# Performance work log

Hardware: AMD Instinct MI355X
Metric: run time of the kernel (lower is better)

## Reference

```python
import jax, jax.numpy as jnp
import numpy as np

N_NODES = 50000
N_EDGES = 600000
D_IN = 128
D_HID = 128
D_OUT = 128
LN_EPS = 1e-5


def _layer_norm(h, g, b):
    mu = jnp.mean(h, axis=-1, keepdims=True)
    var = jnp.var(h, axis=-1, keepdims=True)
    return (h - mu) * jax.lax.rsqrt(var + LN_EPS) * g + b


def _gin_conv(x, src, dst, w1, b1, w2, b2):
    # sum-aggregate neighbor messages at destination nodes, eps = 0
    agg = jax.ops.segment_sum(x[src], dst, num_segments=x.shape[0])
    h = x + agg
    h = jax.nn.relu(h @ w1 + b1)
    return h @ w2 + b2


def setup_inputs() -> dict:
    key = jax.random.key(0)
    ks = jax.random.split(key, 20)
    x = jax.random.normal(ks[0], (N_NODES, D_IN), dtype=jnp.float32)
    edge_index = jax.random.randint(ks[1], (2, N_EDGES), 0, N_NODES, dtype=jnp.int64)
    dims = [(D_IN, D_HID), (D_HID, D_HID), (D_HID, D_HID), (D_HID, D_OUT)]
    inp = {"x": x, "edge_index": edge_index}
    for i, (din, dout) in enumerate(dims):
        s1 = 1.0 / np.sqrt(din)
        s2 = 1.0 / np.sqrt(D_HID)
        inp[f"w1_{i}"] = jax.random.uniform(ks[2 + 4 * i], (din, D_HID), jnp.float32, -s1, s1)
        inp[f"b1_{i}"] = jax.random.uniform(ks[3 + 4 * i], (D_HID,), jnp.float32, -s1, s1)
        inp[f"w2_{i}"] = jax.random.uniform(ks[4 + 4 * i], (D_HID, dout), jnp.float32, -s2, s2)
        inp[f"b2_{i}"] = jax.random.uniform(ks[5 + 4 * i], (dout,), jnp.float32, -s2, s2)
    for i in range(3):  # LayerNorm only on first 3 blocks
        inp[f"g_{i}"] = jnp.ones((D_HID,), jnp.float32)
        inp[f"beta_{i}"] = jnp.zeros((D_HID,), jnp.float32)
    return inp


def reference(x, edge_index,
              w1_0, b1_0, w2_0, b2_0,
              w1_1, b1_1, w2_1, b2_1,
              w1_2, b1_2, w2_2, b2_2,
              w1_3, b1_3, w2_3, b2_3,
              g_0, beta_0, g_1, beta_1, g_2, beta_2):
    src, dst = edge_index[0], edge_index[1]
    mlps = [(w1_0, b1_0, w2_0, b2_0), (w1_1, b1_1, w2_1, b2_1),
            (w1_2, b1_2, w2_2, b2_2), (w1_3, b1_3, w2_3, b2_3)]
    lns = [(g_0, beta_0), (g_1, beta_1), (g_2, beta_2)]
    h = x
    for i in range(3):
        h = _gin_conv(h, src, dst, *mlps[i])
        h = _layer_norm(h, *lns[i])
        h = jax.nn.relu(h)  # dropout rate 0.0 -> identity
    h = _gin_conv(h, src, dst, *mlps[3])  # final block: no norm/act
    return h
```

## Files before the change

kernel.cpp:

```cpp
#include <hip/hip_runtime.h>
#include <hip/hip_bf16.h>

#define NN 50000
#define NE 600000
#define DD 128
#define LDSW 136
#define NB 196
#define BSH 8
#define BSTR 4096
#define EPB 2048
#define NBLK_AC ((NE + EPB - 1) / EPB)

typedef __bf16 bf16;
typedef __attribute__((ext_vector_type(8))) __bf16 bf16x8;
typedef __attribute__((ext_vector_type(4))) float f32x4;
typedef __attribute__((ext_vector_type(4))) unsigned int u32x4;
typedef __attribute__((ext_vector_type(4))) unsigned short u16x4;
typedef unsigned short u16;

__device__ __forceinline__ float bf_lo(unsigned int u) {
    return __builtin_bit_cast(float, u << 16);
}
__device__ __forceinline__ float bf_hi(unsigned int u) {
    return __builtin_bit_cast(float, u & 0xffff0000u);
}
__device__ __forceinline__ unsigned int bf_pack(float x, float y) {
    u16 a = __builtin_bit_cast(u16, (bf16)x);
    u16 b = __builtin_bit_cast(u16, (bf16)y);
    return (unsigned int)a | ((unsigned int)b << 16);
}

struct Ptr8 { const float* p[8]; };

__device__ __forceinline__ int edge_dst(const int* ei, int e, int f) {
    return f ? ei[2 * NE + 2 * e] : ei[NE + e];
}
__device__ __forceinline__ int edge_src(const int* ei, int e, int f) {
    return f ? ei[2 * e] : ei[e];
}

#define J1 (NN * DD / 4)
#define J2 (J1 + 8 * DD * DD)

__global__ __launch_bounds__(256) void k_init(const float* __restrict__ x,
                                              u16* __restrict__ xb,
                                              Ptr8 ws, u16* __restrict__ wt,
                                              int* __restrict__ bcnt,
                                              const int* __restrict__ ei,
                                              int* __restrict__ flag) {
    int tid = threadIdx.x;
    if (blockIdx.x == 0) {
        if (tid == 0) flag[0] = 1;
        __syncthreads();
        if (ei[2 * tid + 1] != 0) flag[0] = 0;
    }
    int id = blockIdx.x * 256 + tid;
    if (id < NB) bcnt[id] = 0;
    if (id < J1) {
        f32x4 v = *(const f32x4*)(x + (size_t)id * 4);
        u16x4 o;
        o.x = __builtin_bit_cast(u16, (bf16)v.x);
        o.y = __builtin_bit_cast(u16, (bf16)v.y);
        o.z = __builtin_bit_cast(u16, (bf16)v.z);
        o.w = __builtin_bit_cast(u16, (bf16)v.w);
        *(u16x4*)(xb + (size_t)id * 4) = o;
    } else if (id < J2) {
        int i = id - J1;
        int m = i >> 14;
        int rem = i & 16383;
        int k = rem >> 7;
        int n = rem & 127;
        bf16 b = (bf16)ws.p[m][k * DD + n];
        wt[(size_t)m * DD * DD + n * DD + k] = __builtin_bit_cast(u16, b);
    }
}

__global__ __launch_bounds__(256) void k_scatter(const int* __restrict__ ei,
                                                 const int* __restrict__ flag,
                                                 int* __restrict__ bcnt,
                                                 unsigned int* __restrict__ tmp) {
    __shared__ int lh[NB];
    __shared__ int gb[NB];
    int tid = threadIdx.x;
    if (tid < NB) lh[tid] = 0;
    __syncthreads();
    int f = flag[0];
    int src[8], dst[8], lp[8];
    bool val[8];
#pragma unroll
    for (int k = 0; k < 8; k++) {
        int e = blockIdx.x * EPB + k * 256 + tid;
        val[k] = (e < NE);
        if (val[k]) {
            src[k] = edge_src(ei, e, f);
            dst[k] = edge_dst(ei, e, f);
            lp[k] = atomicAdd(&lh[dst[k] >> BSH], 1);
        }
    }
    __syncthreads();
    if (tid < NB && lh[tid] > 0) gb[tid] = atomicAdd(&bcnt[tid], lh[tid]);
    __syncthreads();
#pragma unroll
    for (int k = 0; k < 8; k++) {
        if (val[k]) {
            int bkt = dst[k] >> BSH;
            unsigned int pk = (unsigned)src[k] | ((unsigned)(dst[k] & 255) << 16);
            tmp[(size_t)bkt * BSTR + gb[bkt] + lp[k]] = pk;
        }
    }
}

__global__ __launch_bounds__(256) void k_build(const unsigned int* __restrict__ tmp,
                                               const int* __restrict__ bcnt,
                                               int* __restrict__ row_start,
                                               int* __restrict__ adj) {
    __shared__ int cnt[256];
    __shared__ int ccur[256];
    __shared__ int sm[4];
    int b = blockIdx.x, tid = threadIdx.x;
    int base = b << BSH;
    int lane = tid & 63, w = tid >> 6;
    cnt[tid] = 0;
    int v = (tid < b) ? bcnt[tid] : 0;
#pragma unroll
    for (int off = 1; off < 64; off <<= 1) v += __shfl_xor(v, off);
    if (lane == 0) sm[w] = v;
    __syncthreads();
    int G = sm[0] + sm[1] + sm[2] + sm[3];
    int n = bcnt[b];
    size_t ts = (size_t)b * BSTR;
    for (int i = tid; i < n; i += 256) {
        atomicAdd(&cnt[tmp[ts + i] >> 16], 1);
    }
    __syncthreads();
    int v2 = cnt[tid];
    int orig = v2;
#pragma unroll
    for (int off = 1; off < 64; off <<= 1) {
        int t = __shfl_up(v2, off);
        if (lane >= off) v2 += t;
    }
    if (lane == 63) sm[w] = v2;
    __syncthreads();
    int add = 0;
    for (int k = 0; k < w; k++) add += sm[k];
    int ex = G + (v2 - orig) + add;
    ccur[tid] = ex;
    if (base + tid < NN) row_start[base + tid] = ex;
    if (b == 0 && tid == 0) row_start[NN] = NE;
    __syncthreads();
    for (int i = tid; i < n; i += 256) {
        unsigned int pk = tmp[ts + i];
        int p = atomicAdd(&ccur[pk >> 16], 1);
        adj[p] = (int)(pk & 0xffffu);
    }
}

__global__ __launch_bounds__(256) void k_agg(const u16* __restrict__ xb,
                                             const int* __restrict__ row_start,
                                             const int* __restrict__ adj,
                                             u16* __restrict__ out) {
    int gid = blockIdx.x * blockDim.x + threadIdx.x;
    int wave = gid >> 6, lane = gid & 63;
    int grp = lane >> 4, l = lane & 15;
    int node = wave * 4 + grp;
    if (node >= NN) return;
    const u32x4* base = (const u32x4*)xb;
    u32x4 sv = base[(size_t)node * 16 + l];
    float af[8], bf[8];
#pragma unroll
    for (int j = 0; j < 4; j++) {
        af[2 * j] = bf_lo(sv[j]); af[2 * j + 1] = bf_hi(sv[j]);
        bf[2 * j] = 0.f; bf[2 * j + 1] = 0.f;
    }
    int s = row_start[node], e = row_start[node + 1];
    int i = s;
    for (; i + 7 < e; i += 8) {
        u32x4 t0 = base[(size_t)adj[i] * 16 + l];
        u32x4 t1 = base[(size_t)adj[i + 1] * 16 + l];
        u32x4 t2 = base[(size_t)adj[i + 2] * 16 + l];
        u32x4 t3 = base[(size_t)adj[i + 3] * 16 + l];
        u32x4 t4 = base[(size_t)adj[i + 4] * 16 + l];
        u32x4 t5 = base[(size_t)adj[i + 5] * 16 + l];
        u32x4 t6 = base[(size_t)adj[i + 6] * 16 + l];
        u32x4 t7 = base[(size_t)adj[i + 7] * 16 + l];
#pragma unroll
        for (int j = 0; j < 4; j++) {
            af[2 * j]     += (bf_lo(t0[j]) + bf_lo(t1[j])) + (bf_lo(t2[j]) + bf_lo(t3[j]));
            af[2 * j + 1] += (bf_hi(t0[j]) + bf_hi(t1[j])) + (bf_hi(t2[j]) + bf_hi(t3[j]));
            bf[2 * j]     += (bf_lo(t4[j]) + bf_lo(t5[j])) + (bf_lo(t6[j]) + bf_lo(t7[j]));
            bf[2 * j + 1] += (bf_hi(t4[j]) + bf_hi(t5[j])) + (bf_hi(t6[j]) + bf_hi(t7[j]));
        }
    }
    for (; i + 3 < e; i += 4) {
        u32x4 t0 = base[(size_t)adj[i] * 16 + l];
        u32x4 t1 = base[(size_t)adj[i + 1] * 16 + l];
        u32x4 t2 = base[(size_t)adj[i + 2] * 16 + l];
        u32x4 t3 = base[(size_t)adj[i + 3] * 16 + l];
#pragma unroll
        for (int j = 0; j < 4; j++) {
            af[2 * j]     += bf_lo(t0[j]) + bf_lo(t1[j]);
            af[2 * j + 1] += bf_hi(t0[j]) + bf_hi(t1[j]);
            bf[2 * j]     += bf_lo(t2[j]) + bf_lo(t3[j]);
            bf[2 * j + 1] += bf_hi(t2[j]) + bf_hi(t3[j]);
        }
    }
    for (; i < e; i++) {
        u32x4 t = base[(size_t)adj[i] * 16 + l];
#pragma unroll
        for (int j = 0; j < 4; j++) { af[2 * j] += bf_lo(t[j]); af[2 * j + 1] += bf_hi(t[j]); }
    }
    u32x4 o;
#pragma unroll
    for (int j = 0; j < 4; j++) o[j] = bf_pack(af[2 * j] + bf[2 * j], af[2 * j + 1] + bf[2 * j + 1]);
    ((u32x4*)out)[(size_t)node * 16 + l] = o;
}

template <bool LN, bool B16OUT>
__global__ __launch_bounds__(128) void k_mlp(const u16* __restrict__ hin,
                                             const u16* __restrict__ w1t,
                                             const float* __restrict__ b1,
                                             const u16* __restrict__ w2t,
                                             const float* __restrict__ b2,
                                             const float* __restrict__ g,
                                             const float* __restrict__ bta,
                                             void* __restrict__ hout) {
    __shared__ u16 lds[64 * LDSW];
    const int tid = threadIdx.x;
    const int wv = tid >> 6, lane = tid & 63;
    const int l15 = lane & 15, l4 = lane >> 4;
    const int tile0 = blockIdx.x * 64;

    float b1c[8], b2c[8], gc[8], bc[8];
#pragma unroll
    for (int c = 0; c < 8; c++) {
        int col = c * 16 + l15;
        b1c[c] = b1[col];
        b2c[c] = b2[col];
        if (LN) { gc[c] = g[col]; bc[c] = bta[col]; }
    }

#pragma unroll
    for (int it = 0; it < 8; ++it) {
        int slot = tid + it * 128;
        int row = slot >> 4, c16 = slot & 15;
        u32x4 v = {0u, 0u, 0u, 0u};
        int grow = tile0 + row;
        if (grow < NN) v = *(const u32x4*)(hin + (size_t)grow * DD + c16 * 8);
        *(u32x4*)&lds[row * LDSW + c16 * 8] = v;
    }
    __syncthreads();

    f32x4 acc[2][8];
#pragma unroll
    for (int r = 0; r < 2; r++)
#pragma unroll
        for (int c = 0; c < 8; c++) acc[r][c] = (f32x4){0.f, 0.f, 0.f, 0.f};

    const int rowbase = wv * 32;

#pragma unroll
    for (int ks = 0; ks < 4; ++ks) {
        bf16x8 a0 = __builtin_bit_cast(bf16x8,
            *(const u32x4*)&lds[(rowbase + l15) * LDSW + ks * 32 + l4 * 8]);
        bf16x8 a1 = __builtin_bit_cast(bf16x8,
            *(const u32x4*)&lds[(rowbase + 16 + l15) * LDSW + ks * 32 + l4 * 8]);
#pragma unroll
        for (int c = 0; c < 8; c++) {
            bf16x8 b = __builtin_bit_cast(bf16x8,
                *(const u32x4*)(w1t + (size_t)(c * 16 + l15) * DD + ks * 32 + l4 * 8));
            acc[0][c] = __builtin_amdgcn_mfma_f32_16x16x32_bf16(a0, b, acc[0][c], 0, 0, 0);
            acc[1][c] = __builtin_amdgcn_mfma_f32_16x16x32_bf16(a1, b, acc[1][c], 0, 0, 0);
        }
    }

#pragma unroll
    for (int r = 0; r < 2; r++) {
#pragma unroll
        for (int c = 0; c < 8; c++) {
            int col = c * 16 + l15;
#pragma unroll
            for (int j = 0; j < 4; j++) {
                float v = acc[r][c][j] + b1c[c];
                v = v > 0.f ? v : 0.f;
                bf16 b = (bf16)v;
                int row = rowbase + r * 16 + l4 * 4 + j;
                lds[row * LDSW + col] = __builtin_bit_cast(u16, b);
            }
        }
    }

#pragma unroll
    for (int r = 0; r < 2; r++)
#pragma unroll
        for (int c = 0; c < 8; c++) acc[r][c] = (f32x4){0.f, 0.f, 0.f, 0.f};

#pragma unroll
    for (int ks = 0; ks < 4; ++ks) {
        bf16x8 a0 = __builtin_bit_cast(bf16x8,
            *(const u32x4*)&lds[(rowbase + l15) * LDSW + ks * 32 + l4 * 8]);
        bf16x8 a1 = __builtin_bit_cast(bf16x8,
            *(const u32x4*)&lds[(rowbase + 16 + l15) * LDSW + ks * 32 + l4 * 8]);
#pragma unroll
        for (int c = 0; c < 8; c++) {
            bf16x8 b = __builtin_bit_cast(bf16x8,
                *(const u32x4*)(w2t + (size_t)(c * 16 + l15) * DD + ks * 32 + l4 * 8));
            acc[0][c] = __builtin_amdgcn_mfma_f32_16x16x32_bf16(a0, b, acc[0][c], 0, 0, 0);
            acc[1][c] = __builtin_amdgcn_mfma_f32_16x16x32_bf16(a1, b, acc[1][c], 0, 0, 0);
        }
    }

#pragma unroll
    for (int r = 0; r < 2; r++) {
        float vals[8][4];
#pragma unroll
        for (int c = 0; c < 8; c++)
#pragma unroll
            for (int j = 0; j < 4; j++) vals[c][j] = acc[r][c][j] + b2c[c];

        if (LN) {
            float s[4], q[4];
#pragma unroll
            for (int j = 0; j < 4; j++) {
                s[j] = 0.f; q[j] = 0.f;
#pragma unroll
                for (int c = 0; c < 8; c++) {
                    s[j] += vals[c][j];
                    q[j] += vals[c][j] * vals[c][j];
                }
            }
#pragma unroll
            for (int m = 1; m <= 8; m <<= 1) {
#pragma unroll
                for (int j = 0; j < 4; j++) {
                    s[j] += __shfl_xor(s[j], m);
                    q[j] += __shfl_xor(q[j], m);
                }
            }
#pragma unroll
            for (int j = 0; j < 4; j++) {
                float mu = s[j] * (1.f / 128.f);
                float var = q[j] * (1.f / 128.f) - mu * mu;
                float rs = rsqrtf(var + 1e-5f);
#pragma unroll
                for (int c = 0; c < 8; c++) {
                    float v = (vals[c][j] - mu) * rs * gc[c] + bc[c];
                    vals[c][j] = v > 0.f ? v : 0.f;
                }
            }
        }

        if (B16OUT) {
#pragma unroll
            for (int c = 0; c < 8; c++) {
                int col = c * 16 + l15;
#pragma unroll
                for (int j = 0; j < 4; j++) {
                    int row = rowbase + r * 16 + l4 * 4 + j;
                    lds[row * LDSW + col] =
                        __builtin_bit_cast(u16, (bf16)vals[c][j]);
                }
            }
        } else {
#pragma unroll
            for (int c = 0; c < 8; c++) {
                int col = c * 16 + l15;
#pragma unroll
                for (int j = 0; j < 4; j++) {
                    int row = tile0 + rowbase + r * 16 + l4 * 4 + j;
                    if (row < NN)
                        ((float*)hout)[(size_t)row * DD + col] = vals[c][j];
                }
            }
        }
    }

    if (B16OUT) {
#pragma unroll
        for (int it = 0; it < 8; ++it) {
            int slot = it * 64 + lane;
            int row = rowbase + (slot >> 4);
            int c16 = slot & 15;
            u32x4 v = *(const u32x4*)&lds[row * LDSW + c16 * 8];
            int grow = tile0 + row;
            if (grow < NN)
                *(u32x4*)((u16*)hout + (size_t)grow * DD + c16 * 8) = v;
        }
    }
}

extern "C" void kernel_launch(void* const* d_in, const int* in_sizes, int n_in,
                              void* d_out, int out_size, void* d_ws, size_t ws_size,
                              hipStream_t stream) {
    const float* x = (const float*)d_in[0];
    const int* ei = (const int*)d_in[1];
    const float* w1[4]; const float* b1[4]; const float* w2[4]; const float* b2[4];
    for (int i = 0; i < 4; i++) {
        w1[i] = (const float*)d_in[2 + 4 * i];
        b1[i] = (const float*)d_in[3 + 4 * i];
        w2[i] = (const float*)d_in[4 + 4 * i];
        b2[i] = (const float*)d_in[5 + 4 * i];
    }
    const float* g[3]; const float* bt[3];
    for (int i = 0; i < 3; i++) {
        g[i] = (const float*)d_in[18 + 2 * i];
        bt[i] = (const float*)d_in[19 + 2 * i];
    }

    char* ws = (char*)d_ws;
    size_t off = 0;
    auto alloc = [&](size_t bytes) -> char* {
        char* p = ws + off;
        off = (off + bytes + 255) & ~(size_t)255;
        return p;
    };
    int* flag          = (int*)alloc(4);
    int* row_start     = (int*)alloc((NN + 1) * 4);
    int* bcnt          = (int*)alloc(NB * 4);
    int* adj           = (int*)alloc(NE * 4);
    unsigned int* tmp  = (unsigned int*)alloc((size_t)NB * BSTR * 4);
    u16* wt            = (u16*)alloc((size_t)8 * DD * DD * 2);
    u16* xb            = (u16*)alloc((size_t)NN * DD * 2);
    u16* hbf           = (u16*)alloc((size_t)NN * DD * 2);
    u16* hA            = (u16*)alloc((size_t)NN * DD * 2);
    u16* hB            = (u16*)alloc((size_t)NN * DD * 2);

    Ptr8 p8;
    for (int i = 0; i < 4; i++) {
        p8.p[2 * i] = w1[i];
        p8.p[2 * i + 1] = w2[i];
    }

    k_init<<<(J2 + 255) / 256, 256, 0, stream>>>(x, xb, p8, wt, bcnt, ei, flag);
    k_scatter<<<NBLK_AC, 256, 0, stream>>>(ei, flag, bcnt, tmp);
    k_build<<<NB, 256, 0, stream>>>(tmp, bcnt, row_start, adj);

    const int mgrid = (NN + 63) / 64;
    const u16* hin = xb;
    for (int i = 0; i < 4; i++) {
        k_agg<<<(NN / 4 * 64) / 256, 256, 0, stream>>>(hin, row_start, adj, hbf);
        const u16* w1ti = wt + (size_t)(2 * i) * DD * DD;
        const u16* w2ti = wt + (size_t)(2 * i + 1) * DD * DD;
        if (i < 3) {
            u16* outp = (i & 1) ? hB : hA;
            k_mlp<true, true><<<mgrid, 128, 0, stream>>>(
                hbf, w1ti, b1[i], w2ti, b2[i], g[i], bt[i], outp);
            hin = outp;
        } else {
            k_mlp<false, false><<<mgrid, 128, 0, stream>>>(
                hbf, w1ti, b1[i], w2ti, b2[i], nullptr, nullptr, d_out);
        }
    }
}
```

Baseline: 230.9 us.

## Process two row tiles per MLP block with register prefetch of second tile

Each MLP block now handles 128 rows as two 64-row tiles. The second tile's input is prefetched into registers while the first tile's two GEMMs and epilogue run, then copied into a second LDS buffer. The goal is to hide global load latency and halve the grid size, at the cost of more LDS and register pressure and fewer blocks for load balancing.

```diff
diff --git a/kernel.cpp b/kernel.cpp
--- a/kernel.cpp
+++ b/kernel.cpp
@@ -225,11 +225,12 @@
                                              const float* __restrict__ g,
                                              const float* __restrict__ bta,
                                              void* __restrict__ hout) {
-    __shared__ u16 lds[64 * LDSW];
+    __shared__ u16 lds[2][64 * LDSW];
     const int tid = threadIdx.x;
     const int wv = tid >> 6, lane = tid & 63;
     const int l15 = lane & 15, l4 = lane >> 4;
-    const int tile0 = blockIdx.x * 64;
+    const int base0 = blockIdx.x * 128;
+    const int rowbase = wv * 32;
 
     float b1c[8], b2c[8], gc[8], bc[8];
 #pragma unroll
@@ -240,153 +241,176 @@
         if (LN) { gc[c] = g[col]; bc[c] = bta[col]; }
     }
 
+    auto process = [&](u16* L, int t0) {
+        f32x4 acc[2][8];
+#pragma unroll
+        for (int r = 0; r < 2; r++)
+#pragma unroll
+            for (int c = 0; c < 8; c++) acc[r][c] = (f32x4){0.f, 0.f, 0.f, 0.f};
+
+#pragma unroll
+        for (int ks = 0; ks < 4; ++ks) {
+            bf16x8 a0 = __builtin_bit_cast(bf16x8,
+                *(const u32x4*)&L[(rowbase + l15) * LDSW + ks * 32 + l4 * 8]);
+            bf16x8 a1 = __builtin_bit_cast(bf16x8,
+                *(const u32x4*)&L[(rowbase + 16 + l15) * LDSW + ks * 32 + l4 * 8]);
+#pragma unroll
+            for (int c = 0; c < 8; c++) {
+                bf16x8 b = __builtin_bit_cast(bf16x8,
+                    *(const u32x4*)(w1t + (size_t)(c * 16 + l15) * DD + ks * 32 + l4 * 8));
+                acc[0][c] = __builtin_amdgcn_mfma_f32_16x16x32_bf16(a0, b, acc[0][c], 0, 0, 0);
+                acc[1][c] = __builtin_amdgcn_mfma_f32_16x16x32_bf16(a1, b, acc[1][c], 0, 0, 0);
+            }
+        }
+
+#pragma unroll
+        for (int r = 0; r < 2; r++) {
+#pragma unroll
+            for (int c = 0; c < 8; c++) {
+                int col = c * 16 + l15;
+#pragma unroll
+                for (int j = 0; j < 4; j++) {
+                    float v = acc[r][c][j] + b1c[c];
+                    v = v > 0.f ? v : 0.f;
+                    bf16 b = (bf16)v;
+                    int row = rowbase + r * 16 + l4 * 4 + j;
+                    L[row * LDSW + col] = __builtin_bit_cast(u16, b);
+                }
+            }
+        }
+
+#pragma unroll
+        for (int r = 0; r < 2; r++)
+#pragma unroll
+            for (int c = 0; c < 8; c++) acc[r][c] = (f32x4){0.f, 0.f, 0.f, 0.f};
+
+#pragma unroll
+        for (int ks = 0; ks < 4; ++ks) {
+            bf16x8 a0 = __builtin_bit_cast(bf16x8,
+                *(const u32x4*)&L[(rowbase + l15) * LDSW + ks * 32 + l4 * 8]);
+            bf16x8 a1 = __builtin_bit_cast(bf16x8,
+                *(const u32x4*)&L[(rowbase + 16 + l15) * LDSW + ks * 32 + l4 * 8]);
+#pragma unroll
+            for (int c = 0; c < 8; c++) {
+                bf16x8 b = __builtin_bit_cast(bf16x8,
+                    *(const u32x4*)(w2t + (size_t)(c * 16 + l15) * DD + ks * 32 + l4 * 8));
+                acc[0][c] = __builtin_amdgcn_mfma_f32_16x16x32_bf16(a0, b, acc[0][c], 0, 0, 0);
+                acc[1][c] = __builtin_amdgcn_mfma_f32_16x16x32_bf16(a1, b, acc[1][c], 0, 0, 0);
+            }
+        }
+
+#pragma unroll
+        for (int r = 0; r < 2; r++) {
+            float vals[8][4];
+#pragma unroll
+            for (int c = 0; c < 8; c++)
+#pragma unroll
+                for (int j = 0; j < 4; j++) vals[c][j] = acc[r][c][j] + b2c[c];
+
+            if (LN) {
+                float s[4], q[4];
+#pragma unroll
+                for (int j = 0; j < 4; j++) {
+                    s[j] = 0.f; q[j] = 0.f;
+#pragma unroll
+                    for (int c = 0; c < 8; c++) {
+                        s[j] += vals[c][j];
+                        q[j] += vals[c][j] * vals[c][j];
+                    }
+                }
+#pragma unroll
+                for (int m = 1; m <= 8; m <<= 1) {
+#pragma unroll
+                    for (int j = 0; j < 4; j++) {
+                        s[j] += __shfl_xor(s[j], m);
+                        q[j] += __shfl_xor(q[j], m);
+                    }
+                }
+#pragma unroll
+                for (int j = 0; j < 4; j++) {
+                    float mu = s[j] * (1.f / 128.f);
+                    float var = q[j] * (1.f / 128.f) - mu * mu;
+                    float rs = rsqrtf(var + 1e-5f);
+#pragma unroll
+                    for (int c = 0; c < 8; c++) {
+                        float v = (vals[c][j] - mu) * rs * gc[c] + bc[c];
+                        vals[c][j] = v > 0.f ? v : 0.f;
+                    }
+                }
+            }
+
+            if (B16OUT) {
+#pragma unroll
+                for (int c = 0; c < 8; c++) {
+                    int col = c * 16 + l15;
+#pragma unroll
+                    for (int j = 0; j < 4; j++) {
+                        int row = rowbase + r * 16 + l4 * 4 + j;
+                        L[row * LDSW + col] =
+                            __builtin_bit_cast(u16, (bf16)vals[c][j]);
+                    }
+                }
+            } else {
+#pragma unroll
+                for (int c = 0; c < 8; c++) {
+                    int col = c * 16 + l15;
+#pragma unroll
+                    for (int j = 0; j < 4; j++) {
+                        int row = t0 + rowbase + r * 16 + l4 * 4 + j;
+                        if (row < NN)
+                            ((float*)hout)[(size_t)row * DD + col] = vals[c][j];
+                    }
+                }
+            }
+        }
+
+        if (B16OUT) {
+#pragma unroll
+            for (int it = 0; it < 8; ++it) {
+                int slot = it * 64 + lane;
+                int row = rowbase + (slot >> 4);
+                int c16 = slot & 15;
+                u32x4 v = *(const u32x4*)&L[row * LDSW + c16 * 8];
+                int grow = t0 + row;
+                if (grow < NN)
+                    *(u32x4*)((u16*)hout + (size_t)grow * DD + c16 * 8) = v;
+            }
+        }
+    };
+
 #pragma unroll
     for (int it = 0; it < 8; ++it) {
         int slot = tid + it * 128;
         int row = slot >> 4, c16 = slot & 15;
         u32x4 v = {0u, 0u, 0u, 0u};
-        int grow = tile0 + row;
+        int grow = base0 + row;
         if (grow < NN) v = *(const u32x4*)(hin + (size_t)grow * DD + c16 * 8);
-        *(u32x4*)&lds[row * LDSW + c16 * 8] = v;
-    }
-    __syncthreads();
-
-    f32x4 acc[2][8];
-#pragma unroll
-    for (int r = 0; r < 2; r++)
-#pragma unroll
-        for (int c = 0; c < 8; c++) acc[r][c] = (f32x4){0.f, 0.f, 0.f, 0.f};
-
-    const int rowbase = wv * 32;
-
-#pragma unroll
-    for (int ks = 0; ks < 4; ++ks) {
-        bf16x8 a0 = __builtin_bit_cast(bf16x8,
-            *(const u32x4*)&lds[(rowbase + l15) * LDSW + ks * 32 + l4 * 8]);
-        bf16x8 a1 = __builtin_bit_cast(bf16x8,
-            *(const u32x4*)&lds[(rowbase + 16 + l15) * LDSW + ks * 32 + l4 * 8]);
-#pragma unroll
-        for (int c = 0; c < 8; c++) {
-            bf16x8 b = __builtin_bit_cast(bf16x8,
-                *(const u32x4*)(w1t + (size_t)(c * 16 + l15) * DD + ks * 32 + l4 * 8));
-            acc[0][c] = __builtin_amdgcn_mfma_f32_16x16x32_bf16(a0, b, acc[0][c], 0, 0, 0);
-            acc[1][c] = __builtin_amdgcn_mfma_f32_16x16x32_bf16(a1, b, acc[1][c], 0, 0, 0);
-        }
-    }
-
-#pragma unroll
-    for (int r = 0; r < 2; r++) {
-#pragma unroll
-        for (int c = 0; c < 8; c++) {
-            int col = c * 16 + l15;
-#pragma unroll
-            for (int j = 0; j < 4; j++) {
-                float v = acc[r][c][j] + b1c[c];
-                v = v > 0.f ? v : 0.f;
-                bf16 b = (bf16)v;
-                int row = rowbase + r * 16 + l4 * 4 + j;
-                lds[row * LDSW + col] = __builtin_bit_cast(u16, b);
-            }
-        }
-    }
-
-#pragma unroll
-    for (int r = 0; r < 2; r++)
-#pragma unroll
-        for (int c = 0; c < 8; c++) acc[r][c] = (f32x4){0.f, 0.f, 0.f, 0.f};
-
-#pragma unroll
-    for (int ks = 0; ks < 4; ++ks) {
-        bf16x8 a0 = __builtin_bit_cast(bf16x8,
-            *(const u32x4*)&lds[(rowbase + l15) * LDSW + ks * 32 + l4 * 8]);
-        bf16x8 a1 = __builtin_bit_cast(bf16x8,
-            *(const u32x4*)&lds[(rowbase + 16 + l15) * LDSW + ks * 32 + l4 * 8]);
-#pragma unroll
-        for (int c = 0; c < 8; c++) {
-            bf16x8 b = __builtin_bit_cast(bf16x8,
-                *(const u32x4*)(w2t + (size_t)(c * 16 + l15) * DD + ks * 32 + l4 * 8));
-            acc[0][c] = __builtin_amdgcn_mfma_f32_16x16x32_bf16(a0, b, acc[0][c], 0, 0, 0);
-            acc[1][c] = __builtin_amdgcn_mfma_f32_16x16x32_bf16(a1, b, acc[1][c], 0, 0, 0);
-        }
-    }
-
-#pragma unroll
-    for (int r = 0; r < 2; r++) {
-        float vals[8][4];
-#pragma unroll
-        for (int c = 0; c < 8; c++)
-#pragma unroll
-            for (int j = 0; j < 4; j++) vals[c][j] = acc[r][c][j] + b2c[c];
-
-        if (LN) {
-            float s[4], q[4];
-#pragma unroll
-            for (int j = 0; j < 4; j++) {
-                s[j] = 0.f; q[j] = 0.f;
-#pragma unroll
-                for (int c = 0; c < 8; c++) {
-                    s[j] += vals[c][j];
-                    q[j] += vals[c][j] * vals[c][j];
-                }
-            }
-#pragma unroll
-            for (int m = 1; m <= 8; m <<= 1) {
-#pragma unroll
-                for (int j = 0; j < 4; j++) {
-                    s[j] += __shfl_xor(s[j], m);
-                    q[j] += __shfl_xor(q[j], m);
-                }
-            }
-#pragma unroll
-            for (int j = 0; j < 4; j++) {
-                float mu = s[j] * (1.f / 128.f);
-                float var = q[j] * (1.f / 128.f) - mu * mu;
-                float rs = rsqrtf(var + 1e-5f);
-#pragma unroll
-                for (int c = 0; c < 8; c++) {
-                    float v = (vals[c][j] - mu) * rs * gc[c] + bc[c];
-                    vals[c][j] = v > 0.f ? v : 0.f;
-                }
-            }
-        }
-
-        if (B16OUT) {
-#pragma unroll
-            for (int c = 0; c < 8; c++) {
-                int col = c * 16 + l15;
-#pragma unroll
-                for (int j = 0; j < 4; j++) {
-                    int row = rowbase + r * 16 + l4 * 4 + j;
-                    lds[row * LDSW + col] =
-                        __builtin_bit_cast(u16, (bf16)vals[c][j]);
-                }
-            }
-        } else {
-#pragma unroll
-            for (int c = 0; c < 8; c++) {
-                int col = c * 16 + l15;
-#pragma unroll
-                for (int j = 0; j < 4; j++) {
-                    int row = tile0 + rowbase + r * 16 + l4 * 4 + j;
-                    if (row < NN)
-                        ((float*)hout)[(size_t)row * DD + col] = vals[c][j];
-                }
-            }
-        }
-    }
-
-    if (B16OUT) {
-#pragma unroll
-        for (int it = 0; it < 8; ++it) {
-            int slot = it * 64 + lane;
-            int row = rowbase + (slot >> 4);
-            int c16 = slot & 15;
-            u32x4 v = *(const u32x4*)&lds[row * LDSW + c16 * 8];
-            int grow = tile0 + row;
-            if (grow < NN)
-                *(u32x4*)((u16*)hout + (size_t)grow * DD + c16 * 8) = v;
-        }
-    }
+        *(u32x4*)&lds[0][row * LDSW + c16 * 8] = v;
+    }
+    __syncthreads();
+
+    u32x4 pf[8];
+#pragma unroll
+    for (int it = 0; it < 8; ++it) {
+        int slot = tid + it * 128;
+        int row = slot >> 4, c16 = slot & 15;
+        int grow = base0 + 64 + row;
+        u32x4 v = {0u, 0u, 0u, 0u};
+        if (grow < NN) v = *(const u32x4*)(hin + (size_t)grow * DD + c16 * 8);
+        pf[it] = v;
+    }
+
+    process(&lds[0][0], base0);
+
+#pragma unroll
+    for (int it = 0; it < 8; ++it) {
+        int slot = tid + it * 128;
+        int row = slot >> 4, c16 = slot & 15;
+        *(u32x4*)&lds[1][row * LDSW + c16 * 8] = pf[it];
+    }
+    __syncthreads();
+
+    if (base0 + 64 < NN) process(&lds[1][0], base0 + 64);
 }
 
 extern "C" void kernel_launch(void* const* d_in, const int* in_sizes, int n_in,
@@ -435,7 +459,7 @@
     k_scatter<<<NBLK_AC, 256, 0, stream>>>(ei, flag, bcnt, tmp);
     k_build<<<NB, 256, 0, stream>>>(tmp, bcnt, row_start, adj);
 
-    const int mgrid = (NN + 63) / 64;
+    const int mgrid = (NN + 127) / 128;
     const u16* hin = xb;
     for (int i = 0; i < 4; i++) {
         k_agg<<<(NN / 4 * 64) / 256, 256, 0, stream>>>(hin, row_start, adj, hbf);
```

Measured after the change: 246.7 us. 6.9% more time.
